# Performance work log

Hardware: AMD Instinct MI355X
Metric: run time of the kernel (lower is better)

## Reference

```python
import jax, jax.numpy as jnp
import numpy as np

HEADS = 16
DIM_HEAD = 128
DIM = HEADS * DIM_HEAD          # hidden_size = 2048
SEGMENT_LEN = 496
NUM_LONGTERM = 16
NUM_PERSIST = 16
C = SEGMENT_LEN + NUM_LONGTERM  # total_segment_len = 512 (window width)
EPS = 1e-6
THETA = 10000.0
NEG = -jnp.finfo(jnp.float32).max


def _rope(t, cos, sin):
    # t: [b, h, n, d]; cos/sin: [n, d]; interleaved (rotate-half on adjacent pairs)
    t2 = t.reshape(t.shape[:-1] + (DIM_HEAD // 2, 2))
    rot = jnp.stack((-t2[..., 1], t2[..., 0]), axis=-1).reshape(t.shape)
    return t * cos + rot * sin


def _attn_bias():
    # queries: [m_len longterm-mem tokens | segment tokens]
    # keys:    [p_len persistent | m_len longterm-mem | segment tokens]
    q_len = C
    k_len = C + NUM_PERSIST
    pq = NUM_LONGTERM
    pk = NUM_PERSIST + NUM_LONGTERM
    bias = jnp.full((q_len, k_len), NEG, dtype=jnp.float32)
    bias = bias.at[:, :pk].set(0.0)  # everyone attends to the prefix
    sq = q_len - pq
    causal = jnp.tril(jnp.ones((sq, sq), dtype=bool))
    bias = bias.at[pq:, pk:].set(jnp.where(causal, 0.0, NEG))
    return bias


def setup_inputs() -> dict:
    key = jax.random.key(0)
    k1, k2, k3, k4 = jax.random.split(key, 4)
    b, n = 2, 4096  # n must be a multiple of C=512
    return {
        "x": jax.random.normal(k1, (b, n, DIM), dtype=jnp.float32),
        "norm_w": jnp.ones((DIM,), dtype=jnp.float32),
        "w_qkv": jax.random.normal(k2, (3 * DIM, DIM), dtype=jnp.float32) * 0.02,
        "w_out": jax.random.normal(k3, (DIM, DIM), dtype=jnp.float32) * 0.02,
        "pm": jax.random.normal(k4, (2, HEADS, NUM_PERSIST, DIM_HEAD), dtype=jnp.float32) * 0.02,
    }


def reference(x, norm_w, w_qkv, w_out, pm):
    b, n, d = x.shape
    # RMSNorm
    xn = x * jax.lax.rsqrt(jnp.mean(x * x, axis=-1, keepdims=True) + EPS) * norm_w
    # qkv projection (Linear, no bias)
    qkv = xn @ w_qkv.T
    q, k, v = jnp.split(qkv, 3, axis=-1)

    def to_heads(t):  # [b, n, h*d] -> [b, h, n, d]
        return t.reshape(b, n, HEADS, DIM_HEAD).transpose(0, 2, 1, 3)

    q, k, v = to_heads(q), to_heads(k), to_heads(v)

    # RoPE over full sequence positions 0..n-1 (before windowing)
    inv_freq = 1.0 / (THETA ** (jnp.arange(0, DIM_HEAD, 2, dtype=jnp.float32) / DIM_HEAD))
    freqs = jnp.arange(n, dtype=jnp.float32)[:, None] * inv_freq  # [n, d/2]
    freqs = jnp.repeat(freqs, 2, axis=-1)                          # [n, d]
    cos, sin = jnp.cos(freqs), jnp.sin(freqs)
    q = _rope(q, cos, sin)
    k = _rope(k, cos, sin)

    # split into windows of width C: [b, h, n, d] -> [(b*w), h, C, d]
    w = n // C

    def to_windows(t):
        return t.reshape(b, HEADS, w, C, DIM_HEAD).transpose(0, 2, 1, 3, 4).reshape(b * w, HEADS, C, DIM_HEAD)

    q, k, v = to_windows(q), to_windows(k), to_windows(v)

    # prepend persistent memory tokens to k, v
    pmk = jnp.broadcast_to(pm[0], (b * w, HEADS, NUM_PERSIST, DIM_HEAD))
    pmv = jnp.broadcast_to(pm[1], (b * w, HEADS, NUM_PERSIST, DIM_HEAD))
    k = jnp.concatenate((pmk, k), axis=-2)  # [(b*w), h, C+P, d]
    v = jnp.concatenate((pmv, v), axis=-2)

    bias = _attn_bias()  # [C, C+P]
    scale = DIM_HEAD ** -0.5
    sim = jnp.einsum('whqd,whkd->whqk', q, k) * scale + bias
    attn = jax.nn.softmax(sim, axis=-1)
    out = jnp.einsum('whqk,whkd->whqd', attn, v)

    # '(b w) h c d -> b (w c) (h d)'
    out = out.reshape(b, w, HEADS, C, DIM_HEAD).transpose(0, 1, 3, 2, 4).reshape(b, n, HEADS * DIM_HEAD)
    return out @ w_out.T
```

## Files before the change

### kernel.cpp

```cpp
#include <hip/hip_runtime.h>
#include <hip/hip_bf16.h>

typedef __attribute__((ext_vector_type(8))) short short8v;
typedef __attribute__((ext_vector_type(4))) float f32x4;
typedef __attribute__((ext_vector_type(4))) unsigned short us4;
typedef __attribute__((ext_vector_type(4))) unsigned u32x4;

#define DEV static __device__ __forceinline__

DEV unsigned short f2bf(float f) {
  unsigned u = __builtin_bit_cast(unsigned, f);
  u += 0x7FFFu + ((u >> 16) & 1u);
  return (unsigned short)(u >> 16);
}
DEV float bf2f(unsigned short s) {
  unsigned u = ((unsigned)s) << 16;
  return __builtin_bit_cast(float, u);
}
DEV void gload16(const void* g, void* l) {
  __builtin_amdgcn_global_load_lds((const __attribute__((address_space(1))) void*)g,
                                   (__attribute__((address_space(3))) void*)l, 16, 0, 0);
}

__global__ __launch_bounds__(256) void k_prep(const float* __restrict__ w_qkv,
                                              unsigned short* __restrict__ wqkvb,
                                              const float* __restrict__ w_out,
                                              unsigned short* __restrict__ woutb,
                                              const float* __restrict__ pm,
                                              unsigned short* __restrict__ pmk,
                                              unsigned short* __restrict__ vt,
                                              unsigned short* __restrict__ zbuf,
                                              float* __restrict__ ct,
                                              float* __restrict__ st,
                                              const float* __restrict__ x,
                                              const float* __restrict__ norm_w,
                                              unsigned short* __restrict__ xb) {
  __shared__ float red[4];
  const int b = blockIdx.x, tid = threadIdx.x;
  if (b < 12288) {
    long i = (long)b * 256 + tid;
    f32x4 v = *((const f32x4*)w_qkv + i);
    us4 o;
    o[0] = f2bf(v[0]); o[1] = f2bf(v[1]); o[2] = f2bf(v[2]); o[3] = f2bf(v[3]);
    *((us4*)wqkvb + i) = o;
  } else if (b < 16384) {
    long i = (long)(b - 12288) * 256 + tid;
    f32x4 v = *((const f32x4*)w_out + i);
    us4 o;
    o[0] = f2bf(v[0]); o[1] = f2bf(v[1]); o[2] = f2bf(v[2]); o[3] = f2bf(v[3]);
    *((us4*)woutb + i) = o;
  } else if (b < 16512) {
    int idx = (b - 16384) * 256 + tid;
    if (idx < 8) zbuf[idx] = 0;
    int d = idx & 127, p = (idx >> 7) & 15, h = idx >> 11;
    float kvl = pm[((0 * 16 + h) * 16 + p) * 128 + d];
    float vvl = pm[((1 * 16 + h) * 16 + p) * 128 + d];
    pmk[(h * 16 + p) * 128 + d] = f2bf(kvl);
    unsigned short vb = f2bf(vvl);
    for (int w = 0; w < 16; ++w) {
      long base = ((long)(w * 16 + h) * 128 + d) * 576;
      vt[base + p] = vb;
      vt[base + 528 + p] = 0;
      vt[base + 544 + p] = 0;
      vt[base + 560 + p] = 0;
    }
  } else if (b < 17536) {
    int idx = (b - 16512) * 256 + tid;
    int pos = idx >> 6, i = idx & 63;
    float invf = __powf(10000.f, -(float)i * (1.f / 64.f));
    float a = (float)pos * invf;
    ct[idx] = cosf(a);
    st[idx] = sinf(a);
  } else {
    int row = b - 17536;
    const f32x4* xr = (const f32x4*)(x + (long)row * 2048);
    f32x4 v0 = xr[tid * 2], v1 = xr[tid * 2 + 1];
    float ss = v0[0]*v0[0] + v0[1]*v0[1] + v0[2]*v0[2] + v0[3]*v0[3]
             + v1[0]*v1[0] + v1[1]*v1[1] + v1[2]*v1[2] + v1[3]*v1[3];
    ss += __shfl_xor(ss, 1);  ss += __shfl_xor(ss, 2);  ss += __shfl_xor(ss, 4);
    ss += __shfl_xor(ss, 8);  ss += __shfl_xor(ss, 16); ss += __shfl_xor(ss, 32);
    if ((tid & 63) == 0) red[tid >> 6] = ss;
    __syncthreads();
    float tot = red[0] + red[1] + red[2] + red[3];
    float rs = rsqrtf(tot * (1.f / 2048.f) + 1e-6f);
    float xv[8] = {v0[0], v0[1], v0[2], v0[3], v1[0], v1[1], v1[2], v1[3]};
    short8v pack;
#pragma unroll
    for (int j = 0; j < 8; ++j) pack[j] = (short)f2bf(xv[j] * rs * norm_w[tid * 8 + j]);
    *((short8v*)(xb + (long)row * 2048) + tid) = pack;
  }
}


#define VMCNT4 asm volatile("s_waitcnt vmcnt(4)" ::: "memory")
#define VMCNT2 asm volatile("s_waitcnt vmcnt(2)" ::: "memory")
#define VMCNT0 asm volatile("s_waitcnt vmcnt(0)" ::: "memory")
#define SCHEDB __builtin_amdgcn_sched_barrier(0)
#define NOSTG ((void)0)
#define BAR SCHEDB; __builtin_amdgcn_s_barrier(); SCHEDB

template <int OUTF32>
__global__ __launch_bounds__(512, 2) void k_gemm8(const unsigned short* __restrict__ A,
                                                  const unsigned short* __restrict__ B,
                                                  unsigned short* __restrict__ Cb,
                                                  float* __restrict__ Cf,
                                                  int M, int N, int K) {
  __shared__ __align__(16) unsigned short lds[4 * 256 * 64];
  const int tid = threadIdx.x;
  const int lane = tid & 63;
  const int ql = lane & 15, g = lane >> 4;
  const int wid = tid >> 6;
  const int wm = wid >> 2, wn = wid & 3;

  const int nbx = N >> 8;
  const int nwg = gridDim.x;
  int bid = blockIdx.x;
  int bx, by;
  if ((nbx & 7) == 0) {
    const int cpx = nbx >> 3;
    int x = bid & 7, k = bid >> 3;
    bx = x * cpx + (k % cpx);
    by = k / cpx;
  } else {
    int swz = (bid & 7) * (nwg >> 3) + (bid >> 3);
    by = swz / nbx; bx = swz - by * nbx;
  }
  const long rowA0 = (long)by << 8;
  const long rowB0 = (long)bx << 8;

  const int idx0 = tid, idx1 = 512 + tid;
  const int dr0 = idx0 >> 3, sc0 = (idx0 & 7) ^ (dr0 & 7);
  const int dr1 = idx1 >> 3, sc1 = (idx1 & 7) ^ (dr1 & 7);
  const long halfA = 128L * K;
  const unsigned short* pA0 = A + (rowA0 + dr0) * (long)K + sc0 * 8;
  const unsigned short* pA1 = A + (rowA0 + dr1) * (long)K + sc1 * 8;
  const unsigned short* pB0 = B + (rowB0 + dr0) * (long)K + sc0 * 8;
  const unsigned short* pB1 = B + (rowB0 + dr1) * (long)K + sc1 * 8;

  const int rsw0 = (g ^ (ql & 7)) * 8;
  const int rsw1 = ((4 + g) ^ (ql & 7)) * 8;

  short8v faA[4], faB[4], fb[2][4];
  f32x4 acc[8][4] = {};

#define STAGE_A(b, h, kk) do { \
  gload16(pA0 + (long)(h) * halfA + (kk), lds + (b) * 32768 + (h) * 8192 + (idx0 << 3)); \
  gload16(pA1 + (long)(h) * halfA + (kk), lds + (b) * 32768 + (h) * 8192 + (idx1 << 3)); } while (0)
#define STAGE_B(b, h, kk) do { \
  gload16(pB0 + (long)(h) * halfA + (kk), lds + (b) * 32768 + 16384 + (h) * 8192 + (idx0 << 3)); \
  gload16(pB1 + (long)(h) * halfA + (kk), lds + (b) * 32768 + 16384 + (h) * 8192 + (idx1 << 3)); } while (0)

#define RD_FA(dst, buf, mh, ks) do { \
  const unsigned short* p_ = lds + (buf) * 32768 + (((wm << 7) + (mh) * 64 + ql) << 6) + ((ks) ? rsw1 : rsw0); \
  _Pragma("unroll") for (int mi_ = 0; mi_ < 4; ++mi_) dst[mi_] = *(const short8v*)(p_ + (mi_ << 10)); \
} while (0)
#define RD_FB(buf, ks) do { \
  const unsigned short* p_ = lds + (buf) * 32768 + 16384 + (((wn << 6) + ql) << 6) + ((ks) ? rsw1 : rsw0); \
  _Pragma("unroll") for (int n_ = 0; n_ < 4; ++n_) fb[ks][n_] = *(const short8v*)(p_ + (n_ << 10)); \
} while (0)
#define MM(mh, ks, src) do { \
  _Pragma("unroll") for (int mi_ = 0; mi_ < 4; ++mi_) \
    _Pragma("unroll") for (int n_ = 0; n_ < 4; ++n_) \
      acc[(mh) * 4 + mi_][n_] = __builtin_amdgcn_mfma_f32_16x16x32_bf16(src[mi_], fb[ks][n_], acc[(mh) * 4 + mi_][n_], 0, 0, 0); \
} while (0)

#define PH(STG_, PRE_, MM_, VMC_) do { \
  STG_; \
  BAR; \
  __builtin_amdgcn_s_setprio(1); \
  PRE_; \
  MM_; \
  __builtin_amdgcn_s_setprio(0); \
  VMC_; \
  BAR; \
} while (0)

  const int NT = K >> 6;
  const int NITER = NT >> 1;

  STAGE_A(0, 0, 0); STAGE_A(0, 1, 0);
  STAGE_B(0, 0, 0); STAGE_B(0, 1, 0);
  STAGE_B(1, 0, 64); STAGE_B(1, 1, 64);
  VMCNT4;
  BAR;

  for (int i = 0; i < NITER - 1; ++i) {
    const int k1 = (2 * i + 1) << 6;
    const int k2 = (2 * i + 2) << 6;
    const int k3 = (2 * i + 3) << 6;
    RD_FA(faA, 0, 0, 0); RD_FB(0, 0);
    PH(STAGE_A(1, 0, k1), { RD_FA(faB, 0, 0, 1); RD_FB(0, 1); }, MM(0, 0, faA), NOSTG);
    PH(STAGE_A(1, 1, k1), { RD_FA(faA, 0, 1, 0); },             MM(0, 1, faB), NOSTG);
    PH(STAGE_B(0, 0, k2), { RD_FA(faB, 0, 1, 1); },             MM(1, 0, faA), NOSTG);
    PH(STAGE_B(0, 1, k2), {},                                   MM(1, 1, faB), VMCNT4);
    RD_FA(faA, 1, 0, 0); RD_FB(1, 0);
    PH(STAGE_A(0, 0, k2), { RD_FA(faB, 1, 0, 1); RD_FB(1, 1); }, MM(0, 0, faA), NOSTG);
    PH(STAGE_A(0, 1, k2), { RD_FA(faA, 1, 1, 0); },             MM(0, 1, faB), NOSTG);
    PH(STAGE_B(1, 0, k3), { RD_FA(faB, 1, 1, 1); },             MM(1, 0, faA), NOSTG);
    PH(STAGE_B(1, 1, k3), {},                                   MM(1, 1, faB), VMCNT4);
  }
  {
    const int k1 = (NT - 1) << 6;
    RD_FA(faA, 0, 0, 0); RD_FB(0, 0);
    PH(STAGE_A(1, 0, k1), { RD_FA(faB, 0, 0, 1); RD_FB(0, 1); }, MM(0, 0, faA), NOSTG);
    PH(STAGE_A(1, 1, k1), { RD_FA(faA, 0, 1, 0); },             MM(0, 1, faB), NOSTG);
    PH(NOSTG,             { RD_FA(faB, 0, 1, 1); },             MM(1, 0, faA), NOSTG);
    PH(NOSTG,             {},                                   MM(1, 1, faB), VMCNT0);
    RD_FA(faA, 1, 0, 0); RD_FB(1, 0);
    PH(NOSTG,             { RD_FA(faB, 1, 0, 1); RD_FB(1, 1); }, MM(0, 0, faA), NOSTG);
    PH(NOSTG,             { RD_FA(faA, 1, 1, 0); },             MM(0, 1, faB), NOSTG);
    PH(NOSTG,             { RD_FA(faB, 1, 1, 1); },             MM(1, 0, faA), NOSTG);
    PH(NOSTG,             {},                                   MM(1, 1, faB), NOSTG);
  }

#pragma unroll
  for (int am = 0; am < 8; ++am)
#pragma unroll
    for (int n = 0; n < 4; ++n)
#pragma unroll
      for (int r = 0; r < 4; ++r) {
        long row = rowA0 + (wm << 7) + am * 16 + (g << 2) + r;
        long col = rowB0 + (wn << 6) + n * 16 + ql;
        if (OUTF32) Cf[row * N + col] = acc[am][n][r];
        else        Cb[row * N + col] = f2bf(acc[am][n][r]);
      }
#undef STAGE_A
#undef STAGE_B
#undef RD_FA
#undef RD_FB
#undef MM
#undef PH
}

__global__ __launch_bounds__(256) void k_kprep(unsigned short* __restrict__ qkv,
                                               unsigned short* __restrict__ vt,
                                               const float* __restrict__ ct,
                                               const float* __restrict__ st) {
  __shared__ unsigned short lt[64 * 136];
  const int tile = blockIdx.x, h = blockIdx.y;
  const int tid = threadIdx.x;
  const int t0 = tile * 64;
  {
    int row = t0 + (tid >> 2);
    int d0 = (tid & 3) * 32;
    int pos = row & 4095;
    unsigned short* kp = qkv + (long)row * 6144 + 2048 + h * 128 + d0;
    const float* cp = ct + pos * 64 + (d0 >> 1);
    const float* sp = st + pos * 64 + (d0 >> 1);
    f32x4 cv[4], sv[4];
#pragma unroll
    for (int j = 0; j < 4; ++j) { cv[j] = *(const f32x4*)(cp + j * 4); sv[j] = *(const f32x4*)(sp + j * 4); }
    short8v kv[4];
#pragma unroll
    for (int j = 0; j < 4; ++j) kv[j] = *(const short8v*)(kp + j * 8);
#pragma unroll
    for (int j = 0; j < 4; ++j) {
      short8v outv;
#pragma unroll
      for (int p = 0; p < 4; ++p) {
        float a = bf2f((unsigned short)kv[j][2 * p]);
        float b = bf2f((unsigned short)kv[j][2 * p + 1]);
        float c = cv[j][p], s = sv[j][p];
        outv[2 * p]     = (short)f2bf(a * c - b * s);
        outv[2 * p + 1] = (short)f2bf(b * c + a * s);
      }
      *(short8v*)(kp + j * 8) = outv;
    }
  }
  {
    int row = tid >> 2, seg = tid & 3;
    const unsigned short* src = qkv + (long)(t0 + row) * 6144 + 4096 + h * 128 + seg * 32;
#pragma unroll
    for (int j = 0; j < 4; ++j)
      *(short8v*)(lt + row * 136 + seg * 32 + j * 8) = *(const short8v*)(src + j * 8);
  }
  __syncthreads();
  int d = tid >> 1, half = tid & 1;
  int wh = t0 >> 9;
  long dst = ((long)(wh * 16 + h) * 128 + d) * 576 + (t0 & 511) + 16 + half * 32;
  unsigned short tmp[32];
#pragma unroll
  for (int kk = 0; kk < 32; ++kk) tmp[kk] = lt[(half * 32 + kk) * 136 + d];
#pragma unroll
  for (int j = 0; j < 4; ++j) {
    short8v v;
#pragma unroll
    for (int e = 0; e < 8; ++e) v[e] = (short)tmp[j * 8 + e];
    *(short8v*)(vt + dst + j * 8) = v;
  }
}

__global__ __launch_bounds__(512) void k_attn(const unsigned short* __restrict__ qkv,
                                              const unsigned short* __restrict__ vt,
                                              const unsigned short* __restrict__ pmk,
                                              const unsigned short* __restrict__ zbuf,
                                              const float* __restrict__ ct,
                                              const float* __restrict__ stt,
                                              unsigned short* __restrict__ attno) {
  __shared__ __align__(16) unsigned short Ks[3][32 * 128];
  __shared__ __align__(16) unsigned short Vs[3][128 * 32];
  __shared__ unsigned Ps[8][16][16];
  const int wh = blockIdx.x, h = blockIdx.y, qb = blockIdx.z;
  const int tid = threadIdx.x;
  const int wave = tid >> 6, lane = tid & 63;
  const int ql = lane & 15, g = lane >> 4;
  const int tokbase = (wh >> 3) * 4096 + (wh & 7) * 512;
  const int qi = qb * 128 + wave * 16 + ql;
  const int wqmin = qb * 128 + wave * 16;
  const int wqmax = wqmin + 15;
  const long qrow = (long)(tokbase + qi) * 6144;
  const int pos = (tokbase + qi) & 4095;
  short8v qf[4];
#pragma unroll
  for (int ks = 0; ks < 4; ++ks) {
    short8v qv = *(const short8v*)(qkv + qrow + h * 128 + ks * 32 + g * 8);
    f32x4 cv = *(const f32x4*)(ct + pos * 64 + ks * 16 + g * 4);
    f32x4 sv = *(const f32x4*)(stt + pos * 64 + ks * 16 + g * 4);
    const float SC = 0.08838834764831845f;
#pragma unroll
    for (int p = 0; p < 4; ++p) {
      float a = bf2f((unsigned short)qv[2 * p]);
      float b = bf2f((unsigned short)qv[2 * p + 1]);
      qf[ks][2 * p]     = (short)f2bf((a * cv[p] - b * sv[p]) * SC);
      qf[ks][2 * p + 1] = (short)f2bf((b * cv[p] + a * sv[p]) * SC);
    }
  }
  const int nkt = min(17, (qb * 128 + 144 + 31) >> 5);
  const long vbase = (long)(wh * 16 + h) * 128 * 576;

  float mrun = -3.0e38f, lrun = 0.f;
  f32x4 o[8] = {};

#define STAGEKV(kt, b) do { \
    { int kl_ = tid >> 4, dc_ = tid & 15, dcs_ = dc_ ^ (kl_ & 7); \
      int ki_ = (kt) * 32 + kl_; \
      const unsigned short* src_; \
      if (ki_ < 16)       src_ = pmk + (h * 16 + ki_) * 128 + dcs_ * 8; \
      else if (ki_ < 528) src_ = qkv + (long)(tokbase + ki_ - 16) * 6144 + 2048 + h * 128 + dcs_ * 8; \
      else                src_ = zbuf; \
      gload16(src_, &Ks[b][0] + (size_t)tid * 8); } \
    { int d_ = tid >> 2, kc_ = tid & 3, kcs_ = kc_ ^ (d_ & 3); \
      gload16(vt + vbase + (long)d_ * 576 + (kt) * 32 + kcs_ * 8, &Vs[b][0] + (size_t)tid * 8); } \
  } while (0)

  STAGEKV(0, 0);
  STAGEKV(1, 1);
  for (int kt = 0; kt < nkt; ++kt) {
    const int cur = kt % 3;
    SCHEDB; __builtin_amdgcn_s_barrier(); SCHEDB;
    if (kt + 2 < nkt) STAGEKV(kt + 2, (kt + 2) % 3);
    if (kt + 2 < nkt)      VMCNT4;
    else if (kt + 1 < nkt) VMCNT2;
    else                   VMCNT0;
    SCHEDB;
    if (kt * 32 <= wqmax + 16) {
      f32x4 stv[2] = {};
      __builtin_amdgcn_s_setprio(1);
#pragma unroll
      for (int kf = 0; kf < 2; ++kf) {
        int row = kf * 16 + ql;
#pragma unroll
        for (int ks = 0; ks < 4; ++ks) {
          int chunk = (ks * 4 + g) ^ (row & 7);
          short8v kv = *(const short8v*)(&Ks[cur][0] + row * 128 + chunk * 8);
          stv[kf] = __builtin_amdgcn_mfma_f32_16x16x32_bf16(kv, qf[ks], stv[kf], 0, 0, 0);
        }
      }
      __builtin_amdgcn_s_setprio(0);
      float tmax = -3.0e38f;
      const bool needmask = !(kt == 0 || (kt * 32 + 15 <= wqmin));
      if (needmask) {
#pragma unroll
        for (int kf = 0; kf < 2; ++kf)
#pragma unroll
          for (int r = 0; r < 4; ++r) {
            int ki = kt * 32 + kf * 16 + g * 4 + r;
            bool ok = (ki < 32) || (qi >= 16 && ki <= qi + 16);
            float s = ok ? stv[kf][r] : -3.0e38f;
            stv[kf][r] = s;
            tmax = fmaxf(tmax, s);
          }
      } else {
#pragma unroll
        for (int kf = 0; kf < 2; ++kf)
#pragma unroll
          for (int r = 0; r < 4; ++r) tmax = fmaxf(tmax, stv[kf][r]);
      }
      tmax = fmaxf(tmax, __shfl_xor(tmax, 16));
      tmax = fmaxf(tmax, __shfl_xor(tmax, 32));
      if (!__all(tmax <= mrun + 8.f)) {
        float mnew = fmaxf(mrun, tmax);
        float corr = __expf(mrun - mnew);
        lrun *= corr;
#pragma unroll
        for (int db = 0; db < 8; ++db) {
          o[db][0] *= corr; o[db][1] *= corr; o[db][2] *= corr; o[db][3] *= corr;
        }
        mrun = mnew;
      }
#pragma unroll
      for (int kf = 0; kf < 2; ++kf)
#pragma unroll
        for (int r = 0; r < 4; ++r) {
          float p = __expf(stv[kf][r] - mrun);
          stv[kf][r] = p;
          lrun += p;
        }
#pragma unroll
      for (int kf = 0; kf < 2; ++kf) {
        unsigned w01 = (unsigned)f2bf(stv[kf][0]) | ((unsigned)f2bf(stv[kf][1]) << 16);
        unsigned w23 = (unsigned)f2bf(stv[kf][2]) | ((unsigned)f2bf(stv[kf][3]) << 16);
        int pr = kf * 8 + 2 * g;
        Ps[wave][pr][ql ^ (pr & 7)] = w01;
        Ps[wave][pr + 1][ql ^ ((pr + 1) & 7)] = w23;
      }
      u32x4 pbw;
#pragma unroll
      for (int t = 0; t < 4; ++t) {
        int pr = 4 * g + t;
        pbw[t] = Ps[wave][pr][ql ^ (pr & 7)];
      }
      short8v pb = __builtin_bit_cast(short8v, pbw);
      __builtin_amdgcn_s_setprio(1);
#pragma unroll
      for (int db = 0; db < 8; ++db) {
        int d = db * 16 + ql;
        int kc = g ^ (d & 3);
        short8v vf = *(const short8v*)(&Vs[cur][0] + d * 32 + kc * 8);
        o[db] = __builtin_amdgcn_mfma_f32_16x16x32_bf16(vf, pb, o[db], 0, 0, 0);
      }
      __builtin_amdgcn_s_setprio(0);
    }
  }
#undef STAGEKV
  lrun += __shfl_xor(lrun, 16);
  lrun += __shfl_xor(lrun, 32);
  float inv = 1.0f / lrun;
  long obase = (long)(tokbase + qi) * 2048 + h * 128;
#pragma unroll
  for (int db = 0; db < 8; ++db) {
    us4 ov;
#pragma unroll
    for (int r = 0; r < 4; ++r) ov[r] = f2bf(o[db][r] * inv);
    *(us4*)(attno + obase + db * 16 + g * 4) = ov;
  }
}

extern "C" void kernel_launch(void* const* d_in, const int* in_sizes, int n_in,
                              void* d_out, int out_size, void* d_ws, size_t ws_size,
                              hipStream_t stream) {
  const float* x      = (const float*)d_in[0];
  const float* norm_w = (const float*)d_in[1];
  const float* w_qkv  = (const float*)d_in[2];
  const float* w_out  = (const float*)d_in[3];
  const float* pm     = (const float*)d_in[4];
  float* out = (float*)d_out;

  char* ws = (char*)d_ws;
  size_t off = 0;
  auto alloc = [&](size_t bytes) -> void* {
    void* p = ws + off;
    off += (bytes + 255) & ~(size_t)255;
    return p;
  };
  unsigned short* xb    = (unsigned short*)alloc(8192ull * 2048 * 2);
  unsigned short* wqkvb = (unsigned short*)alloc(6144ull * 2048 * 2);
  unsigned short* woutb = (unsigned short*)alloc(2048ull * 2048 * 2);
  unsigned short* qkv   = (unsigned short*)alloc(8192ull * 6144 * 2);
  unsigned short* vt    = (unsigned short*)alloc(256ull * 128 * 576 * 2);
  unsigned short* attno = (unsigned short*)alloc(8192ull * 2048 * 2);
  unsigned short* pmk   = (unsigned short*)alloc(16 * 16 * 128 * 2);
  float* ct             = (float*)alloc(4096 * 64 * 4);
  float* stt            = (float*)alloc(4096 * 64 * 4);
  unsigned short* zbuf  = (unsigned short*)alloc(256);

  hipLaunchKernelGGL(k_prep, dim3(25728), dim3(256), 0, stream,
                     w_qkv, wqkvb, w_out, woutb, pm, pmk, vt, zbuf, ct, stt, x, norm_w, xb);
  hipLaunchKernelGGL((k_gemm8<0>), dim3(24 * 32), dim3(512), 0, stream,
                     xb, wqkvb, qkv, (float*)nullptr, 8192, 6144, 2048);
  hipLaunchKernelGGL(k_kprep, dim3(128, 16), dim3(256), 0, stream, qkv, vt, ct, stt);
  hipLaunchKernelGGL(k_attn, dim3(16, 16, 4), dim3(512), 0, stream,
                     qkv, vt, pmk, zbuf, ct, stt, attno);
  hipLaunchKernelGGL((k_gemm8<1>), dim3(8 * 32), dim3(512), 0, stream,
                     attno, woutb, (unsigned short*)nullptr, out, 8192, 2048, 2048);
}
```

Measured before the change: 395.1 us.

## Replace phased ping-pong GEMM schedule with simple double-buffered loop

Replaces the hand-interleaved eight-phase GEMM main loop with a plain double-buffered loop. In the old loop, global-to-LDS stages, LDS fragment reads and MFMA blocks were split across barriers. The new loop issues all loads for the next K tile at once, waits for the current tile, then runs all fragment reads and MFMAs for that tile. This cuts the number of barriers and reuses a single A-fragment register set, which may lower register pressure. The cost is coarser overlap: LDS reads are no longer hidden behind MFMAs and load issue is bunched, so latency hiding may get worse.

```diff
diff --git a/kernel.cpp b/kernel.cpp
--- a/kernel.cpp
+++ b/kernel.cpp
@@ -92,11 +92,9 @@
 }
 
 
-#define VMCNT4 asm volatile("s_waitcnt vmcnt(4)" ::: "memory")
-#define VMCNT2 asm volatile("s_waitcnt vmcnt(2)" ::: "memory")
+#define VMCNT8 asm volatile("s_waitcnt vmcnt(8)" ::: "memory")
 #define VMCNT0 asm volatile("s_waitcnt vmcnt(0)" ::: "memory")
 #define SCHEDB __builtin_amdgcn_sched_barrier(0)
-#define NOSTG ((void)0)
 #define BAR SCHEDB; __builtin_amdgcn_s_barrier(); SCHEDB
 
 template <int OUTF32>
@@ -140,7 +138,7 @@
   const int rsw0 = (g ^ (ql & 7)) * 8;
   const int rsw1 = ((4 + g) ^ (ql & 7)) * 8;
 
-  short8v faA[4], faB[4], fb[2][4];
+  short8v fa[4], fb[2][4];
   f32x4 acc[8][4] = {};
 
 #define STAGE_A(b, h, kk) do { \
@@ -150,67 +148,46 @@
   gload16(pB0 + (long)(h) * halfA + (kk), lds + (b) * 32768 + 16384 + (h) * 8192 + (idx0 << 3)); \
   gload16(pB1 + (long)(h) * halfA + (kk), lds + (b) * 32768 + 16384 + (h) * 8192 + (idx1 << 3)); } while (0)
 
-#define RD_FA(dst, buf, mh, ks) do { \
+#define RD_FA(buf, mh, ks) do { \
   const unsigned short* p_ = lds + (buf) * 32768 + (((wm << 7) + (mh) * 64 + ql) << 6) + ((ks) ? rsw1 : rsw0); \
-  _Pragma("unroll") for (int mi_ = 0; mi_ < 4; ++mi_) dst[mi_] = *(const short8v*)(p_ + (mi_ << 10)); \
+  _Pragma("unroll") for (int mi_ = 0; mi_ < 4; ++mi_) fa[mi_] = *(const short8v*)(p_ + (mi_ << 10)); \
 } while (0)
 #define RD_FB(buf, ks) do { \
   const unsigned short* p_ = lds + (buf) * 32768 + 16384 + (((wn << 6) + ql) << 6) + ((ks) ? rsw1 : rsw0); \
   _Pragma("unroll") for (int n_ = 0; n_ < 4; ++n_) fb[ks][n_] = *(const short8v*)(p_ + (n_ << 10)); \
 } while (0)
-#define MM(mh, ks, src) do { \
+#define MM(mh, ks) do { \
   _Pragma("unroll") for (int mi_ = 0; mi_ < 4; ++mi_) \
     _Pragma("unroll") for (int n_ = 0; n_ < 4; ++n_) \
-      acc[(mh) * 4 + mi_][n_] = __builtin_amdgcn_mfma_f32_16x16x32_bf16(src[mi_], fb[ks][n_], acc[(mh) * 4 + mi_][n_], 0, 0, 0); \
+      acc[(mh) * 4 + mi_][n_] = __builtin_amdgcn_mfma_f32_16x16x32_bf16(fa[mi_], fb[ks][n_], acc[(mh) * 4 + mi_][n_], 0, 0, 0); \
 } while (0)
 
-#define PH(STG_, PRE_, MM_, VMC_) do { \
-  STG_; \
-  BAR; \
-  __builtin_amdgcn_s_setprio(1); \
-  PRE_; \
-  MM_; \
-  __builtin_amdgcn_s_setprio(0); \
-  VMC_; \
-  BAR; \
-} while (0)
-
   const int NT = K >> 6;
-  const int NITER = NT >> 1;
 
   STAGE_A(0, 0, 0); STAGE_A(0, 1, 0);
   STAGE_B(0, 0, 0); STAGE_B(0, 1, 0);
-  STAGE_B(1, 0, 64); STAGE_B(1, 1, 64);
-  VMCNT4;
-  BAR;
-
-  for (int i = 0; i < NITER - 1; ++i) {
-    const int k1 = (2 * i + 1) << 6;
-    const int k2 = (2 * i + 2) << 6;
-    const int k3 = (2 * i + 3) << 6;
-    RD_FA(faA, 0, 0, 0); RD_FB(0, 0);
-    PH(STAGE_A(1, 0, k1), { RD_FA(faB, 0, 0, 1); RD_FB(0, 1); }, MM(0, 0, faA), NOSTG);
-    PH(STAGE_A(1, 1, k1), { RD_FA(faA, 0, 1, 0); },             MM(0, 1, faB), NOSTG);
-    PH(STAGE_B(0, 0, k2), { RD_FA(faB, 0, 1, 1); },             MM(1, 0, faA), NOSTG);
-    PH(STAGE_B(0, 1, k2), {},                                   MM(1, 1, faB), VMCNT4);
-    RD_FA(faA, 1, 0, 0); RD_FB(1, 0);
-    PH(STAGE_A(0, 0, k2), { RD_FA(faB, 1, 0, 1); RD_FB(1, 1); }, MM(0, 0, faA), NOSTG);
-    PH(STAGE_A(0, 1, k2), { RD_FA(faA, 1, 1, 0); },             MM(0, 1, faB), NOSTG);
-    PH(STAGE_B(1, 0, k3), { RD_FA(faB, 1, 1, 1); },             MM(1, 0, faA), NOSTG);
-    PH(STAGE_B(1, 1, k3), {},                                   MM(1, 1, faB), VMCNT4);
-  }
-  {
-    const int k1 = (NT - 1) << 6;
-    RD_FA(faA, 0, 0, 0); RD_FB(0, 0);
-    PH(STAGE_A(1, 0, k1), { RD_FA(faB, 0, 0, 1); RD_FB(0, 1); }, MM(0, 0, faA), NOSTG);
-    PH(STAGE_A(1, 1, k1), { RD_FA(faA, 0, 1, 0); },             MM(0, 1, faB), NOSTG);
-    PH(NOSTG,             { RD_FA(faB, 0, 1, 1); },             MM(1, 0, faA), NOSTG);
-    PH(NOSTG,             {},                                   MM(1, 1, faB), VMCNT0);
-    RD_FA(faA, 1, 0, 0); RD_FB(1, 0);
-    PH(NOSTG,             { RD_FA(faB, 1, 0, 1); RD_FB(1, 1); }, MM(0, 0, faA), NOSTG);
-    PH(NOSTG,             { RD_FA(faA, 1, 1, 0); },             MM(0, 1, faB), NOSTG);
-    PH(NOSTG,             { RD_FA(faB, 1, 1, 1); },             MM(1, 0, faA), NOSTG);
-    PH(NOSTG,             {},                                   MM(1, 1, faB), NOSTG);
+
+  for (int kt = 0; kt < NT; ++kt) {
+    const int cur = kt & 1;
+    BAR;
+    if (kt + 1 < NT) {
+      const int kk = (kt + 1) << 6;
+      STAGE_A(cur ^ 1, 0, kk); STAGE_A(cur ^ 1, 1, kk);
+      STAGE_B(cur ^ 1, 0, kk); STAGE_B(cur ^ 1, 1, kk);
+      VMCNT8;
+    } else {
+      VMCNT0;
+    }
+    BAR;
+    __builtin_amdgcn_s_setprio(1);
+    RD_FB(cur, 0);
+    RD_FB(cur, 1);
+#pragma unroll
+    for (int mh = 0; mh < 2; ++mh) {
+      RD_FA(cur, mh, 0); MM(mh, 0);
+      RD_FA(cur, mh, 1); MM(mh, 1);
+    }
+    __builtin_amdgcn_s_setprio(0);
   }
 
 #pragma unroll
@@ -229,7 +206,6 @@
 #undef RD_FA
 #undef RD_FB
 #undef MM
-#undef PH
 }
 
 __global__ __launch_bounds__(256) void k_kprep(unsigned short* __restrict__ qkv,
@@ -289,6 +265,9 @@
     *(short8v*)(vt + dst + j * 8) = v;
   }
 }
+
+#define VMCNT4 asm volatile("s_waitcnt vmcnt(4)" ::: "memory")
+#define VMCNT2 asm volatile("s_waitcnt vmcnt(2)" ::: "memory")
 
 __global__ __launch_bounds__(512) void k_attn(const unsigned short* __restrict__ qkv,
                                               const unsigned short* __restrict__ vt,
@@ -347,7 +326,7 @@
   STAGEKV(1, 1);
   for (int kt = 0; kt < nkt; ++kt) {
     const int cur = kt % 3;
-    SCHEDB; __builtin_amdgcn_s_barrier(); SCHEDB;
+    BAR;
     if (kt + 2 < nkt) STAGEKV(kt + 2, (kt + 2) % 3);
     if (kt + 2 < nkt)      VMCNT4;
     else if (kt + 1 < nkt) VMCNT2;
```

Result: slower. 411.9 us (+4.3%).
